# Optimization experiments

Measured on AMD Instinct MI355X. Metric: run time of the kernel, lower is better.

## Reference

```python
import jax, jax.numpy as jnp
import numpy as np

C = 128  # n_atom_basis


def setup_inputs() -> dict:
    key = jax.random.key(0)
    k_h, k_A, k_Ww, k_Wb, k_aw, k_ab = jax.random.split(key, 6)
    B, N = 8, 2048
    h = jax.random.normal(k_h, (B, N, C), dtype=jnp.float32)
    A = jax.random.uniform(k_A, (B, N, N), dtype=jnp.float32)
    # nn.Linear(C, C)
    lim_W = 1.0 / np.sqrt(C)
    W_w = jax.random.uniform(k_Ww, (C, C), minval=-lim_W, maxval=lim_W, dtype=jnp.float32)
    W_b = jax.random.uniform(k_Wb, (C,), minval=-lim_W, maxval=lim_W, dtype=jnp.float32)
    # nn.Linear(2C, 1)
    lim_a = 1.0 / np.sqrt(2 * C)
    a_w = jax.random.uniform(k_aw, (2 * C,), minval=-lim_a, maxval=lim_a, dtype=jnp.float32)
    a_b = jax.random.uniform(k_ab, (), minval=-lim_a, maxval=lim_a, dtype=jnp.float32)
    return {"h": h, "A": A, "W_w": W_w, "W_b": W_b, "a_w": a_w, "a_b": a_b}


def reference(h, A, W_w, W_b, a_w, a_b):
    # Wh computed once ([B,N,C]) instead of the original's redundant [B,N,N,C] broadcast.
    Wh = jnp.einsum('bnc,dc->bnd', h, W_w) + W_b
    # a([hi, hj]) = a_w[:C]@Wh_i + a_w[C:]@Wh_j + a_b  -> rank-1 decomposition of the concat-linear
    si = Wh @ a_w[:C]          # [B,N]
    sj = Wh @ a_w[C:]          # [B,N]
    s = si[:, :, None] + sj[:, None, :] + a_b  # [B,N,N] raw scores
    e = jnp.exp(s) * A                          # masked exp (no max-subtraction: matches original math)
    alpha = e / jnp.sum(e, axis=2, keepdims=True)
    # weighted sum over neighbors j of the ORIGINAL h (as in the source, not Wh)
    h_prime = jnp.einsum('bij,bjc->bic', alpha, h)
    return h_prime
```

## Files before the change

kernel.cpp:

```cpp
#include <hip/hip_runtime.h>
#include <math.h>
#include <stdint.h>

#define Bn 8
#define Nn 2048
#define Cn 128
#define CP 144
#define NKB (Nn / 32)

typedef _Float16 f16x8 __attribute__((ext_vector_type(8)));
typedef _Float16 f16x4 __attribute__((ext_vector_type(4)));
typedef _Float16 f16x2 __attribute__((ext_vector_type(2)));
typedef __fp16   fp16x2 __attribute__((ext_vector_type(2)));
typedef float    f32x4 __attribute__((ext_vector_type(4)));

__global__ __launch_bounds__(256) void rows_kernel(const float* __restrict__ h,
                                                   const float* __restrict__ Ww,
                                                   const float* __restrict__ Wb,
                                                   const float* __restrict__ aw,
                                                   _Float16* __restrict__ hWt) {
    __shared__ float tile[16][132];
    __shared__ float vlo[128];
    __shared__ float vhi[128];
    __shared__ float wsh[16];
    __shared__ float b2sh;

    int bid = blockIdx.x;
    int b   = bid & 7;
    int n0  = (bid >> 3) << 4;
    int tid = threadIdx.x;

    {
        int c = tid & 127, half = tid >> 7;
        float acc = 0.f;
#pragma unroll
        for (int dd = 0; dd < 64; ++dd) {
            int d = half * 64 + dd;
            acc += Ww[d * Cn + c] * aw[Cn + d];
        }
        if (half) vhi[c] = acc; else vlo[c] = acc;
    }
    if (tid < 64) {
        float b2p = Wb[tid] * aw[Cn + tid] + Wb[tid + 64] * aw[Cn + tid + 64];
        b2p += __shfl_xor(b2p, 32, 64);
        b2p += __shfl_xor(b2p, 16, 64);
        b2p += __shfl_xor(b2p, 8, 64);
        b2p += __shfl_xor(b2p, 4, 64);
        b2p += __shfl_xor(b2p, 2, 64);
        b2p += __shfl_xor(b2p, 1, 64);
        if (tid == 0) b2sh = b2p;
    }
    {
#pragma unroll
        for (int i = 0; i < 2; ++i) {
            int idx = tid + 256 * i;
            int r = idx >> 5, f4 = idx & 31;
            *(float4*)&tile[r][f4 * 4] =
                ((const float4*)(h + (size_t)(b * Nn + n0 + r) * Cn))[f4];
        }
    }
    __syncthreads();

    {
        int r = tid >> 4, g = tid & 15;
        float acc = 0.f;
#pragma unroll
        for (int ii = 0; ii < 8; ++ii) {
            int i = g * 8 + ii;
            acc += tile[r][i] * (vlo[i] + vhi[i]);
        }
        acc += __shfl_xor(acc, 1, 64);
        acc += __shfl_xor(acc, 2, 64);
        acc += __shfl_xor(acc, 4, 64);
        acc += __shfl_xor(acc, 8, 64);
        if (g == 0) wsh[r] = expf(acc + b2sh);
    }
    __syncthreads();

    {
        int kb = n0 >> 5, khalf = (n0 >> 4) & 1;
        _Float16* hWb = hWt + ((size_t)(b * NKB + kb) * CP) * 32 + khalf * 16;
#pragma unroll
        for (int i = 0; i < 5; ++i) {
            int idx = tid + 256 * i;
            if (idx < 1152) {
                int cp = idx >> 3, p = idx & 7;
                int r0 = p * 2;
                f16x2 v2;
                if (cp < 128) {
                    v2[0] = (_Float16)(wsh[r0] * tile[r0][cp]);
                    v2[1] = (_Float16)(wsh[r0 + 1] * tile[r0 + 1][cp]);
                } else if (cp == 128) {
                    v2[0] = (_Float16)wsh[r0];
                    v2[1] = (_Float16)wsh[r0 + 1];
                } else {
                    v2[0] = (_Float16)0.f;
                    v2[1] = (_Float16)0.f;
                }
                *(f16x2*)(hWb + (size_t)cp * 32 + p * 2) = v2;
            }
        }
    }
}

__global__ __launch_bounds__(512, 4) void attn_kernel(const float* __restrict__ A,
                                                      const _Float16* __restrict__ hWt,
                                                      float* __restrict__ out) {
    __shared__ _Float16 Af[2][2][32][40];
    __shared__ float den[32];

    int bid = blockIdx.x;
    int b   = bid & 7;
    int i0  = (bid >> 3) << 5;
    int tid = threadIdx.x;
    int wv  = tid >> 6, l = tid & 63;
    int m   = l & 15, q = l >> 4;

    const float*    Ab  = A   + (size_t)(b * Nn + i0) * Nn;
    const _Float16* hWb = hWt + (size_t)b * NKB * CP * 32;

    int sr = tid >> 4, sf4 = tid & 15;
    const float* sg = Ab + (size_t)sr * Nn + sf4 * 4;
    int sch = sf4 >> 3, skl = (sf4 & 7) * 4;

    f32x4 accc[2];
    f32x4 acc8;
    accc[0] = (f32x4){0.f, 0.f, 0.f, 0.f};
    accc[1] = (f32x4){0.f, 0.f, 0.f, 0.f};
    acc8    = (f32x4){0.f, 0.f, 0.f, 0.f};

    auto loadA = [&](int t) { return *(const float4*)(sg + t * 64); };
    auto storeA = [&](int t, float4 v) {
        union { fp16x2 h2[2]; f16x4 v4; } u;
        u.h2[0] = __builtin_amdgcn_cvt_pkrtz(v.x, v.y);
        u.h2[1] = __builtin_amdgcn_cvt_pkrtz(v.z, v.w);
        *(f16x4*)&Af[t & 1][sch][sr][skl] = u.v4;
    };
    auto loadB = [&](int t, f16x8* bf) {
#pragma unroll
        for (int ck = 0; ck < 2; ++ck)
            bf[ck] = *(const f16x8*)(hWb + ((size_t)(2 * t + ck) * CP + wv * 16 + m) * 32 + q * 8);
        if (wv < 2) {
#pragma unroll
            for (int ck = 0; ck < 2; ++ck)
                bf[2 + ck] = *(const f16x8*)(hWb + ((size_t)(2 * t + ck) * CP + 128 + m) * 32 + q * 8);
        }
    };
    auto compute = [&](int buf, const f16x8* bf) {
#pragma unroll
        for (int ck = 0; ck < 2; ++ck) {
            f16x8 af0 = *(const f16x8*)&Af[buf][ck][m][q * 8];
            f16x8 af1 = *(const f16x8*)&Af[buf][ck][16 + m][q * 8];
            accc[0] = __builtin_amdgcn_mfma_f32_16x16x32_f16(af0, bf[ck], accc[0], 0, 0, 0);
            accc[1] = __builtin_amdgcn_mfma_f32_16x16x32_f16(af1, bf[ck], accc[1], 0, 0, 0);
            if (wv < 2)
                acc8 = __builtin_amdgcn_mfma_f32_16x16x32_f16(wv ? af1 : af0, bf[2 + ck],
                                                              acc8, 0, 0, 0);
        }
    };

    float4 a0 = loadA(0);
    float4 a1 = loadA(1);
    f16x8 bfA[4], bfB[4];
    loadB(0, bfA);
    storeA(0, a0);
    __syncthreads();

    for (int t2 = 0; t2 < 16; ++t2) {
        int te = 2 * t2, to = te + 1;
        loadB(to, bfB);
        if (t2 < 15) a0 = loadA(te + 2);
        compute(0, bfA);
        storeA(to, a1);
        __syncthreads();
        if (t2 < 15) {
            loadB(to + 1, bfA);
            a1 = loadA(to + 2);
        }
        compute(1, bfB);
        if (t2 < 15) storeA(to + 1, a0);
        __syncthreads();
    }

    if (wv < 2 && m == 0) {
#pragma unroll
        for (int r = 0; r < 4; ++r) den[wv * 16 + q * 4 + r] = acc8[r];
    }
    __syncthreads();

#pragma unroll
    for (int mt = 0; mt < 2; ++mt) {
#pragma unroll
        for (int r = 0; r < 4; ++r) {
            int row = mt * 16 + q * 4 + r;
            float invd = 1.f / den[row];
            out[(size_t)(b * Nn + i0 + row) * Cn + wv * 16 + m] = accc[mt][r] * invd;
        }
    }
}

extern "C" void kernel_launch(void* const* d_in, const int* in_sizes, int n_in,
                              void* d_out, int out_size, void* d_ws, size_t ws_size,
                              hipStream_t stream) {
    const float* h  = (const float*)d_in[0];
    const float* A  = (const float*)d_in[1];
    const float* Ww = (const float*)d_in[2];
    const float* Wb = (const float*)d_in[3];
    const float* aw = (const float*)d_in[4];
    float* out = (float*)d_out;

    _Float16* hWt = (_Float16*)d_ws;

    rows_kernel<<<Bn * (Nn / 16), 256, 0, stream>>>(h, Ww, Wb, aw, hWt);
    attn_kernel<<<Bn * (Nn / 32), 512, 0, stream>>>(A, hWt, out);
}
```

Before: 222.5 us.

## Double K-step per stage and compute softmax denominator with VALU dot products

Each pipeline stage now covers 128 columns of A instead of 64, so there are half as many stages and barriers, and each thread loads 8 floats per stage. The denominator is no longer computed by extra MFMAs on waves 0-1 using the padded weight column. Instead, each thread does a VALU dot product of its converted A chunk with the exp-weight column and reduces it with shuffles. This evens out work across waves and removes the divergent MFMA path, at the cost of more LDS, more registers and some extra VALU work.

```diff
diff --git a/kernel.cpp b/kernel.cpp
--- a/kernel.cpp
+++ b/kernel.cpp
@@ -7,6 +7,7 @@
 #define Cn 128
 #define CP 144
 #define NKB (Nn / 32)
+#define NPH (Nn / 128)
 
 typedef _Float16 f16x8 __attribute__((ext_vector_type(8)));
 typedef _Float16 f16x4 __attribute__((ext_vector_type(4)));
@@ -106,7 +107,7 @@
 __global__ __launch_bounds__(512, 4) void attn_kernel(const float* __restrict__ A,
                                                       const _Float16* __restrict__ hWt,
                                                       float* __restrict__ out) {
-    __shared__ _Float16 Af[2][2][32][40];
+    __shared__ __align__(16) _Float16 Af[2][4][32][40];
     __shared__ float den[32];
 
     int bid = blockIdx.x;
@@ -120,72 +121,82 @@
     const _Float16* hWb = hWt + (size_t)b * NKB * CP * 32;
 
     int sr = tid >> 4, sf4 = tid & 15;
-    const float* sg = Ab + (size_t)sr * Nn + sf4 * 4;
-    int sch = sf4 >> 3, skl = (sf4 & 7) * 4;
+    const float* sg = Ab + (size_t)sr * Nn + sf4 * 8;
+    int sch = sf4 >> 2, skl = (sf4 & 3) * 8;
+    const _Float16* wg = hWb + ((size_t)sch * CP + 128) * 32 + skl;
 
     f32x4 accc[2];
-    f32x4 acc8;
     accc[0] = (f32x4){0.f, 0.f, 0.f, 0.f};
     accc[1] = (f32x4){0.f, 0.f, 0.f, 0.f};
-    acc8    = (f32x4){0.f, 0.f, 0.f, 0.f};
-
-    auto loadA = [&](int t) { return *(const float4*)(sg + t * 64); };
-    auto storeA = [&](int t, float4 v) {
-        union { fp16x2 h2[2]; f16x4 v4; } u;
-        u.h2[0] = __builtin_amdgcn_cvt_pkrtz(v.x, v.y);
-        u.h2[1] = __builtin_amdgcn_cvt_pkrtz(v.z, v.w);
-        *(f16x4*)&Af[t & 1][sch][sr][skl] = u.v4;
+    float dacc = 0.f;
+
+    auto loadA = [&](int t, float4* a) {
+        a[0] = *(const float4*)(sg + (size_t)t * 128);
+        a[1] = *(const float4*)(sg + (size_t)t * 128 + 4);
+    };
+    auto loadW = [&](int t) {
+        return *(const f16x8*)(wg + (size_t)(4 * t) * CP * 32);
+    };
+    auto storeA = [&](int t, const float4* a, f16x8 wf) {
+        union { fp16x2 h2[4]; f16x8 v8; } u;
+        u.h2[0] = __builtin_amdgcn_cvt_pkrtz(a[0].x, a[0].y);
+        u.h2[1] = __builtin_amdgcn_cvt_pkrtz(a[0].z, a[0].w);
+        u.h2[2] = __builtin_amdgcn_cvt_pkrtz(a[1].x, a[1].y);
+        u.h2[3] = __builtin_amdgcn_cvt_pkrtz(a[1].z, a[1].w);
+        *(f16x8*)&Af[t & 1][sch][sr][skl] = u.v8;
+        float s = 0.f;
+#pragma unroll
+        for (int i = 0; i < 8; ++i)
+            s += (float)u.v8[i] * (float)wf[i];
+        dacc += s;
     };
     auto loadB = [&](int t, f16x8* bf) {
 #pragma unroll
-        for (int ck = 0; ck < 2; ++ck)
-            bf[ck] = *(const f16x8*)(hWb + ((size_t)(2 * t + ck) * CP + wv * 16 + m) * 32 + q * 8);
-        if (wv < 2) {
-#pragma unroll
-            for (int ck = 0; ck < 2; ++ck)
-                bf[2 + ck] = *(const f16x8*)(hWb + ((size_t)(2 * t + ck) * CP + 128 + m) * 32 + q * 8);
-        }
+        for (int j = 0; j < 4; ++j)
+            bf[j] = *(const f16x8*)(hWb + ((size_t)(4 * t + j) * CP + wv * 16 + m) * 32 + q * 8);
     };
     auto compute = [&](int buf, const f16x8* bf) {
 #pragma unroll
-        for (int ck = 0; ck < 2; ++ck) {
-            f16x8 af0 = *(const f16x8*)&Af[buf][ck][m][q * 8];
-            f16x8 af1 = *(const f16x8*)&Af[buf][ck][16 + m][q * 8];
-            accc[0] = __builtin_amdgcn_mfma_f32_16x16x32_f16(af0, bf[ck], accc[0], 0, 0, 0);
-            accc[1] = __builtin_amdgcn_mfma_f32_16x16x32_f16(af1, bf[ck], accc[1], 0, 0, 0);
-            if (wv < 2)
-                acc8 = __builtin_amdgcn_mfma_f32_16x16x32_f16(wv ? af1 : af0, bf[2 + ck],
-                                                              acc8, 0, 0, 0);
-        }
-    };
-
-    float4 a0 = loadA(0);
-    float4 a1 = loadA(1);
-    f16x8 bfA[4], bfB[4];
+        for (int j = 0; j < 4; ++j) {
+            f16x8 af0 = *(const f16x8*)&Af[buf][j][m][q * 8];
+            f16x8 af1 = *(const f16x8*)&Af[buf][j][16 + m][q * 8];
+            accc[0] = __builtin_amdgcn_mfma_f32_16x16x32_f16(af0, bf[j], accc[0], 0, 0, 0);
+            accc[1] = __builtin_amdgcn_mfma_f32_16x16x32_f16(af1, bf[j], accc[1], 0, 0, 0);
+        }
+    };
+
+    float4 a0[2], a1[2];
+    f16x8 bfA[4], bfB[4], wfA, wfB;
+    loadA(0, a0);
+    loadA(1, a1);
     loadB(0, bfA);
-    storeA(0, a0);
-    __syncthreads();
-
-    for (int t2 = 0; t2 < 16; ++t2) {
+    wfA = loadW(0);
+    storeA(0, a0, wfA);
+    __syncthreads();
+
+    for (int t2 = 0; t2 < NPH / 2; ++t2) {
         int te = 2 * t2, to = te + 1;
         loadB(to, bfB);
-        if (t2 < 15) a0 = loadA(te + 2);
+        wfB = loadW(to);
+        if (t2 < NPH / 2 - 1) loadA(te + 2, a0);
         compute(0, bfA);
-        storeA(to, a1);
+        storeA(to, a1, wfB);
         __syncthreads();
-        if (t2 < 15) {
+        if (t2 < NPH / 2 - 1) {
             loadB(to + 1, bfA);
-            a1 = loadA(to + 2);
+            wfA = loadW(to + 1);
+            loadA(to + 2, a1);
         }
         compute(1, bfB);
-        if (t2 < 15) storeA(to + 1, a0);
+        if (t2 < NPH / 2 - 1) storeA(to + 1, a0, wfA);
         __syncthreads();
     }
 
-    if (wv < 2 && m == 0) {
-#pragma unroll
-        for (int r = 0; r < 4; ++r) den[wv * 16 + q * 4 + r] = acc8[r];
-    }
+    dacc += __shfl_xor(dacc, 1, 64);
+    dacc += __shfl_xor(dacc, 2, 64);
+    dacc += __shfl_xor(dacc, 4, 64);
+    dacc += __shfl_xor(dacc, 8, 64);
+    if (sf4 == 0) den[sr] = dacc;
     __syncthreads();
 
 #pragma unroll
```

Measured after the change: 231.6 us. 4.1% more time.

## Load A fragments directly from global into registers, removing LDS staging

Applied to the files above, without the earlier changes.

Each wave now reads its A fragments for the MFMA directly from global memory, converting to fp16 in registers and double-buffering them. This removes the shared-memory tile and the two barriers per iteration. In exchange, all eight waves in a block redundantly fetch the same A rows, so reads of A through the caches grow several-fold and register pressure rises.

```diff
diff --git a/kernel.cpp b/kernel.cpp
--- a/kernel.cpp
+++ b/kernel.cpp
@@ -106,7 +106,6 @@
 __global__ __launch_bounds__(512, 4) void attn_kernel(const float* __restrict__ A,
                                                       const _Float16* __restrict__ hWt,
                                                       float* __restrict__ out) {
-    __shared__ _Float16 Af[2][2][32][40];
     __shared__ float den[32];
 
     int bid = blockIdx.x;
@@ -116,12 +115,9 @@
     int wv  = tid >> 6, l = tid & 63;
     int m   = l & 15, q = l >> 4;
 
-    const float*    Ab  = A   + (size_t)(b * Nn + i0) * Nn;
+    const float* pA0 = A + (size_t)(b * Nn + i0 + m) * Nn + q * 8;
+    const float* pA1 = pA0 + (size_t)16 * Nn;
     const _Float16* hWb = hWt + (size_t)b * NKB * CP * 32;
-
-    int sr = tid >> 4, sf4 = tid & 15;
-    const float* sg = Ab + (size_t)sr * Nn + sf4 * 4;
-    int sch = sf4 >> 3, skl = (sf4 & 7) * 4;
 
     f32x4 accc[2];
     f32x4 acc8;
@@ -129,12 +125,25 @@
     accc[1] = (f32x4){0.f, 0.f, 0.f, 0.f};
     acc8    = (f32x4){0.f, 0.f, 0.f, 0.f};
 
-    auto loadA = [&](int t) { return *(const float4*)(sg + t * 64); };
-    auto storeA = [&](int t, float4 v) {
-        union { fp16x2 h2[2]; f16x4 v4; } u;
-        u.h2[0] = __builtin_amdgcn_cvt_pkrtz(v.x, v.y);
-        u.h2[1] = __builtin_amdgcn_cvt_pkrtz(v.z, v.w);
-        *(f16x4*)&Af[t & 1][sch][sr][skl] = u.v4;
+    auto loadAraw = [&](int t, float4* r) {
+        const float* p0 = pA0 + t * 64;
+        const float* p1 = pA1 + t * 64;
+        r[0] = *(const float4*)(p0);
+        r[1] = *(const float4*)(p0 + 4);
+        r[2] = *(const float4*)(p0 + 32);
+        r[3] = *(const float4*)(p0 + 36);
+        r[4] = *(const float4*)(p1);
+        r[5] = *(const float4*)(p1 + 4);
+        r[6] = *(const float4*)(p1 + 32);
+        r[7] = *(const float4*)(p1 + 36);
+    };
+    auto cvt8 = [&](float4 x, float4 y) {
+        union { fp16x2 h2[4]; f16x8 v8; } u;
+        u.h2[0] = __builtin_amdgcn_cvt_pkrtz(x.x, x.y);
+        u.h2[1] = __builtin_amdgcn_cvt_pkrtz(x.z, x.w);
+        u.h2[2] = __builtin_amdgcn_cvt_pkrtz(y.x, y.y);
+        u.h2[3] = __builtin_amdgcn_cvt_pkrtz(y.z, y.w);
+        return u.v8;
     };
     auto loadB = [&](int t, f16x8* bf) {
 #pragma unroll
@@ -146,40 +155,41 @@
                 bf[2 + ck] = *(const f16x8*)(hWb + ((size_t)(2 * t + ck) * CP + 128 + m) * 32 + q * 8);
         }
     };
-    auto compute = [&](int buf, const f16x8* bf) {
-#pragma unroll
-        for (int ck = 0; ck < 2; ++ck) {
-            f16x8 af0 = *(const f16x8*)&Af[buf][ck][m][q * 8];
-            f16x8 af1 = *(const f16x8*)&Af[buf][ck][16 + m][q * 8];
-            accc[0] = __builtin_amdgcn_mfma_f32_16x16x32_f16(af0, bf[ck], accc[0], 0, 0, 0);
-            accc[1] = __builtin_amdgcn_mfma_f32_16x16x32_f16(af1, bf[ck], accc[1], 0, 0, 0);
-            if (wv < 2)
-                acc8 = __builtin_amdgcn_mfma_f32_16x16x32_f16(wv ? af1 : af0, bf[2 + ck],
-                                                              acc8, 0, 0, 0);
-        }
-    };
-
-    float4 a0 = loadA(0);
-    float4 a1 = loadA(1);
-    f16x8 bfA[4], bfB[4];
-    loadB(0, bfA);
-    storeA(0, a0);
-    __syncthreads();
+    auto mfmas = [&](f16x8 a00, f16x8 a01, f16x8 a10, f16x8 a11, const f16x8* bf) {
+        accc[0] = __builtin_amdgcn_mfma_f32_16x16x32_f16(a00, bf[0], accc[0], 0, 0, 0);
+        accc[1] = __builtin_amdgcn_mfma_f32_16x16x32_f16(a10, bf[0], accc[1], 0, 0, 0);
+        if (wv < 2)
+            acc8 = __builtin_amdgcn_mfma_f32_16x16x32_f16(wv ? a10 : a00, bf[2], acc8, 0, 0, 0);
+        accc[0] = __builtin_amdgcn_mfma_f32_16x16x32_f16(a01, bf[1], accc[0], 0, 0, 0);
+        accc[1] = __builtin_amdgcn_mfma_f32_16x16x32_f16(a11, bf[1], accc[1], 0, 0, 0);
+        if (wv < 2)
+            acc8 = __builtin_amdgcn_mfma_f32_16x16x32_f16(wv ? a11 : a01, bf[3], acc8, 0, 0, 0);
+    };
+
+    float4 Ra[8], Rb[8];
+    f16x8 bf[4];
+    loadAraw(0, Ra);
 
     for (int t2 = 0; t2 < 16; ++t2) {
         int te = 2 * t2, to = te + 1;
-        loadB(to, bfB);
-        if (t2 < 15) a0 = loadA(te + 2);
-        compute(0, bfA);
-        storeA(to, a1);
-        __syncthreads();
-        if (t2 < 15) {
-            loadB(to + 1, bfA);
-            a1 = loadA(to + 2);
-        }
-        compute(1, bfB);
-        if (t2 < 15) storeA(to + 1, a0);
-        __syncthreads();
+        loadB(te, bf);
+        {
+            f16x8 a00 = cvt8(Ra[0], Ra[1]);
+            f16x8 a01 = cvt8(Ra[2], Ra[3]);
+            f16x8 a10 = cvt8(Ra[4], Ra[5]);
+            f16x8 a11 = cvt8(Ra[6], Ra[7]);
+            loadAraw(to, Rb);
+            mfmas(a00, a01, a10, a11, bf);
+        }
+        loadB(to, bf);
+        {
+            f16x8 a00 = cvt8(Rb[0], Rb[1]);
+            f16x8 a01 = cvt8(Rb[2], Rb[3]);
+            f16x8 a10 = cvt8(Rb[4], Rb[5]);
+            f16x8 a11 = cvt8(Rb[6], Rb[7]);
+            if (t2 < 15) loadAraw(te + 2, Ra);
+            mfmas(a00, a01, a10, a11, bf);
+        }
     }
 
     if (wv < 2 && m == 0) {
```

After: 317.2 us. +42.5%, slower.
